# Kernel optimization log

Measured on AMD Instinct MI355X. Metric: run time of the kernel, lower is better.

The kernel has to match this reference:

```python
import jax, jax.numpy as jnp
import numpy as np

EPS = 1e-5

def setup_inputs() -> dict:
    key = jax.random.key(0)
    k1, k2 = jax.random.split(key)
    N, D = 8192, 256
    q_features = jax.random.normal(k1, (N, D), dtype=jnp.float32)
    g_features = jax.random.normal(k2, (N, D), dtype=jnp.float32)
    return {"q_features": q_features, "g_features": g_features}

def reference(q_features, g_features):
    # logits[i, j] = q_i . g_j ; original computes row i as g_features @ q_i
    logits = jnp.einsum('id,jd->ij', q_features, g_features)  # [N, N]
    # exp(l_ii)/sum_j exp(l_ij) == softmax row diagonal (stable form, same math)
    probs_diag = jnp.diagonal(jax.nn.softmax(logits, axis=-1))  # [N]
    loss = jnp.mean(-jnp.log(probs_diag + EPS))
    return loss
```

## Files before the change

### kernel.cpp

```cpp
#include <hip/hip_runtime.h>
#include <stdint.h>


#define LOG2E 1.44269504f
#define KOFF  92.3324826f

typedef __attribute__((ext_vector_type(4))) float f32x4;
typedef __attribute__((ext_vector_type(4))) int   i32x4;
typedef __attribute__((ext_vector_type(8))) int   i32x8;

typedef __attribute__((address_space(1))) const uint32_t gu32;
typedef __attribute__((address_space(3))) uint32_t lu32;

static __device__ __forceinline__ i32x8 cat8(i32x4 lo, i32x4 hi) {
    i32x8 r;
    r[0] = lo[0]; r[1] = lo[1]; r[2] = lo[2]; r[3] = lo[3];
    r[4] = hi[0]; r[5] = hi[1]; r[6] = hi[2]; r[7] = hi[3];
    return r;
}

__global__ __launch_bounds__(256) void k_cvt(const float* __restrict__ q,
                                             const float* __restrict__ g,
                                             char* __restrict__ qb,
                                             char* __restrict__ gb) {
    int o = blockIdx.x * 256 + threadIdx.x;
    const float* src = q;
    char* dst = qb;
    float sc = LOG2E;
    if (o >= 262144) { o -= 262144; src = g; dst = gb; sc = 1.0f; }
    int row = o >> 5, slot = o & 31;
    const float4* sp = (const float4*)(src + row * 256 + slot * 8);
    float4 a = sp[0], b = sp[1];
    uint32_t w0 = __builtin_amdgcn_cvt_pk_fp8_f32(a.x * sc, a.y * sc, 0, false);
    w0 = __builtin_amdgcn_cvt_pk_fp8_f32(a.z * sc, a.w * sc, w0, true);
    uint32_t w1 = __builtin_amdgcn_cvt_pk_fp8_f32(b.x * sc, b.y * sc, 0, false);
    w1 = __builtin_amdgcn_cvt_pk_fp8_f32(b.z * sc, b.w * sc, w1, true);
    int p = row >> 6, cf = (row >> 4) & 3, l15 = row & 15;
    int kb = slot >> 4;
    int gi = slot & 15;
    int quad = gi >> 2;
    int j = gi & 3;
    uint2 wv; wv.x = w0; wv.y = w1;
    *(uint2*)(dst + (size_t)p * 16384 + ((kb * 4 + cf) << 11)
              + ((j >> 1) << 10) + (quad * 16 + l15) * 16 + (j & 1) * 8) = wv;
}

__global__ __launch_bounds__(512, 2) void k_main(const char* __restrict__ qb,
                                                 const char* __restrict__ gb,
                                                 float* __restrict__ zpart,
                                                 float* __restrict__ diag) {
    __shared__ char lds[16384];
    const int tid  = threadIdx.x;
    const int wave = tid >> 6;
    const int lane = tid & 63;
    const int l15  = lane & 15;
    const int quad = lane >> 4;
    const int h2   = wave & 1;
    const int t    = blockIdx.x >> 5;
    const int cs   = blockIdx.x & 31;
    const int rowbase = t * 256 + wave * 32;

    i32x8 afrag[2][2];
    {
        const char* qp = qb + (size_t)(t * 4 + (wave >> 1)) * 16384 + lane * 16;
#pragma unroll
        for (int rg = 0; rg < 2; ++rg)
#pragma unroll
            for (int kb = 0; kb < 2; ++kb) {
                const char* tp = qp + ((kb * 4 + h2 * 2 + rg) << 11);
                afrag[rg][kb] = cat8(*(const i32x4*)tp, *(const i32x4*)(tp + 1024));
            }
    }

    float zacc[2][4];
#pragma unroll
    for (int rg = 0; rg < 2; ++rg)
#pragma unroll
        for (int r = 0; r < 4; ++r) zacc[rg][r] = 0.f;

    const bool bd = (t == cs);

    for (int jt = 0; jt < 4; ++jt) {
        const char* gp = gb + (size_t)(cs * 4 + jt) * 16384;
#pragma unroll
        for (int i = 0; i < 2; ++i) {
            int c = wave * 2 + i;
            __builtin_amdgcn_global_load_lds(
                (gu32*)(gp + (c << 10) + (lane << 4)),
                (lu32*)(lds + (c << 10)), 16, 0, 0);
        }
        __syncthreads();

        const bool dg = bd && (jt == (wave >> 1));
#pragma unroll
        for (int cf = 0; cf < 4; ++cf) {
            f32x4 acc[2];
#pragma unroll
            for (int rg = 0; rg < 2; ++rg)
                acc[rg] = (f32x4){-KOFF, -KOFF, -KOFF, -KOFF};
#pragma unroll
            for (int kb = 0; kb < 2; ++kb) {
                const char* bp = lds + ((kb * 4 + cf) << 11) + lane * 16;
                i32x8 b = cat8(*(const i32x4*)bp, *(const i32x4*)(bp + 1024));
#pragma unroll
                for (int rg = 0; rg < 2; ++rg)
                    acc[rg] = __builtin_amdgcn_mfma_scale_f32_16x16x128_f8f6f4(
                        afrag[rg][kb], b, acc[rg],
                        0, 0,
                        0, 0x7f7f7f7f,
                        0, 0x7f7f7f7f);
            }
#pragma unroll
            for (int rg = 0; rg < 2; ++rg)
#pragma unroll
                for (int r = 0; r < 4; ++r)
                    zacc[rg][r] += __builtin_amdgcn_exp2f(acc[rg][r]);
            if (dg) {
                int rgd = cf - h2 * 2;
                if (rgd >= 0 && rgd < 2) {
#pragma unroll
                    for (int r = 0; r < 4; ++r)
                        if (quad * 4 + r == l15)
                            diag[rowbase + rgd * 16 + l15] = acc[rgd][r];
                }
            }
        }
        __syncthreads();
    }

#pragma unroll
    for (int d = 1; d < 16; d <<= 1)
#pragma unroll
        for (int rg = 0; rg < 2; ++rg)
#pragma unroll
            for (int r = 0; r < 4; ++r)
                zacc[rg][r] += __shfl_xor(zacc[rg][r], d, 64);

    if (l15 == 0) {
#pragma unroll
        for (int rg = 0; rg < 2; ++rg)
#pragma unroll
            for (int r = 0; r < 4; ++r)
                zpart[(rowbase + rg * 16 + quad * 4 + r) * 32 + cs] = zacc[rg][r];
    }
}

__global__ __launch_bounds__(256) void k_fin1(const float* __restrict__ zpart,
                                              const float* __restrict__ diag,
                                              float* __restrict__ partial) {
    __shared__ float red[4];
    int r = blockIdx.x * 256 + threadIdx.x;
    const float4* z = (const float4*)(zpart + r * 32);
    float Z = 0.f;
#pragma unroll
    for (int i = 0; i < 8; ++i) {
        float4 a = z[i];
        Z += (a.x + a.y) + (a.z + a.w);
    }
    float p = __builtin_amdgcn_exp2f(diag[r]) / Z;
    float v = -logf(p + 1e-5f);
#pragma unroll
    for (int dd = 1; dd < 64; dd <<= 1) v += __shfl_xor(v, dd, 64);
    if ((threadIdx.x & 63) == 0) red[threadIdx.x >> 6] = v;
    __syncthreads();
    if (threadIdx.x == 0)
        partial[blockIdx.x] = (red[0] + red[1]) + (red[2] + red[3]);
}

__global__ void k_fin2(const float* __restrict__ partial, float* __restrict__ out) {
    float v = (threadIdx.x < 32) ? partial[threadIdx.x] : 0.f;
#pragma unroll
    for (int d = 1; d < 32; d <<= 1) v += __shfl_xor(v, d, 64);
    if (threadIdx.x == 0) out[0] = v * (1.f / 8192.f);
}

extern "C" void kernel_launch(void* const* d_in, const int* in_sizes, int n_in,
                              void* d_out, int out_size, void* d_ws, size_t ws_size,
                              hipStream_t stream) {
    const float* q = (const float*)d_in[0];
    const float* g = (const float*)d_in[1];
    char* ws = (char*)d_ws;
    char*  qb     = ws;
    char*  gb     = ws + (2u << 20);
    float* diag   = (float*)(ws + (4u << 20));
    float* zpart  = (float*)(ws + (4u << 20) + (32u << 10));
    float* partial= (float*)(ws + (4u << 20) + (1056u << 10));
    k_cvt <<<2048, 256, 0, stream>>>(q, g, qb, gb);
    k_main<<<1024, 512, 0, stream>>>(qb, gb, zpart, diag);
    k_fin1<<<32,   256, 0, stream>>>(zpart, diag, partial);
    k_fin2<<<1,     64, 0, stream>>>(partial, (float*)d_out);
    (void)in_sizes; (void)n_in; (void)out_size; (void)ws_size;
}
```

Measured before the change: 96.17 us.

## Double-buffer LDS tiles in main kernel and merge final reduction kernels

Doubles the shared-memory buffer in the main GEMM+exp kernel so the next g tile's global-to-LDS load is issued before computing on the current tile, overlapping load latency with MFMA work and dropping one barrier per iteration. The two tail reduction kernels are merged into one using an atomic counter, reset in the conversion kernel, so the last block performs the final sum. This removes one kernel launch. LDS use per block doubles to 32KB, which may affect occupancy at two blocks per CU.

```diff
diff --git a/kernel.cpp b/kernel.cpp
--- a/kernel.cpp
+++ b/kernel.cpp
@@ -22,7 +22,9 @@
 __global__ __launch_bounds__(256) void k_cvt(const float* __restrict__ q,
                                              const float* __restrict__ g,
                                              char* __restrict__ qb,
-                                             char* __restrict__ gb) {
+                                             char* __restrict__ gb,
+                                             unsigned* __restrict__ counter) {
+    if (blockIdx.x == 0 && threadIdx.x == 0) *counter = 0u;
     int o = blockIdx.x * 256 + threadIdx.x;
     const float* src = q;
     char* dst = qb;
@@ -49,7 +51,7 @@
                                                  const char* __restrict__ gb,
                                                  float* __restrict__ zpart,
                                                  float* __restrict__ diag) {
-    __shared__ char lds[16384];
+    __shared__ char lds[2][16384];
     const int tid  = threadIdx.x;
     const int wave = tid >> 6;
     const int lane = tid & 63;
@@ -80,18 +82,28 @@
 
     const bool bd = (t == cs);
 
+    const char* gbase = gb + (size_t)(cs * 4) * 16384;
+#define STAGE(JT, BUF)                                                        \
+    {                                                                         \
+        const char* gp = gbase + (size_t)(JT) * 16384;                        \
+        _Pragma("unroll")                                                     \
+        for (int i = 0; i < 2; ++i) {                                         \
+            int c = wave * 2 + i;                                             \
+            __builtin_amdgcn_global_load_lds(                                 \
+                (gu32*)(gp + (c << 10) + (lane << 4)),                        \
+                (lu32*)(&lds[BUF][0] + (c << 10)), 16, 0, 0);                 \
+        }                                                                     \
+    }
+
+    STAGE(0, 0);
+    __syncthreads();
+    int cur = 0;
+
     for (int jt = 0; jt < 4; ++jt) {
-        const char* gp = gb + (size_t)(cs * 4 + jt) * 16384;
-#pragma unroll
-        for (int i = 0; i < 2; ++i) {
-            int c = wave * 2 + i;
-            __builtin_amdgcn_global_load_lds(
-                (gu32*)(gp + (c << 10) + (lane << 4)),
-                (lu32*)(lds + (c << 10)), 16, 0, 0);
-        }
-        __syncthreads();
+        if (jt < 3) STAGE(jt + 1, cur ^ 1);
 
         const bool dg = bd && (jt == (wave >> 1));
+        const char* lbase = &lds[cur][0];
 #pragma unroll
         for (int cf = 0; cf < 4; ++cf) {
             f32x4 acc[2];
@@ -100,7 +112,7 @@
                 acc[rg] = (f32x4){-KOFF, -KOFF, -KOFF, -KOFF};
 #pragma unroll
             for (int kb = 0; kb < 2; ++kb) {
-                const char* bp = lds + ((kb * 4 + cf) << 11) + lane * 16;
+                const char* bp = lbase + ((kb * 4 + cf) << 11) + lane * 16;
                 i32x8 b = cat8(*(const i32x4*)bp, *(const i32x4*)(bp + 1024));
 #pragma unroll
                 for (int rg = 0; rg < 2; ++rg)
@@ -125,8 +137,12 @@
                 }
             }
         }
-        __syncthreads();
-    }
+        if (jt < 3) {
+            __syncthreads();
+            cur ^= 1;
+        }
+    }
+#undef STAGE
 
 #pragma unroll
     for (int d = 1; d < 16; d <<= 1)
@@ -145,10 +161,13 @@
     }
 }
 
-__global__ __launch_bounds__(256) void k_fin1(const float* __restrict__ zpart,
-                                              const float* __restrict__ diag,
-                                              float* __restrict__ partial) {
+__global__ __launch_bounds__(256) void k_fin(const float* __restrict__ zpart,
+                                             const float* __restrict__ diag,
+                                             float* __restrict__ partial,
+                                             unsigned* __restrict__ counter,
+                                             float* __restrict__ out) {
     __shared__ float red[4];
+    __shared__ int lastflag;
     int r = blockIdx.x * 256 + threadIdx.x;
     const float4* z = (const float4*)(zpart + r * 32);
     float Z = 0.f;
@@ -163,15 +182,26 @@
     for (int dd = 1; dd < 64; dd <<= 1) v += __shfl_xor(v, dd, 64);
     if ((threadIdx.x & 63) == 0) red[threadIdx.x >> 6] = v;
     __syncthreads();
-    if (threadIdx.x == 0)
-        partial[blockIdx.x] = (red[0] + red[1]) + (red[2] + red[3]);
-}
-
-__global__ void k_fin2(const float* __restrict__ partial, float* __restrict__ out) {
-    float v = (threadIdx.x < 32) ? partial[threadIdx.x] : 0.f;
-#pragma unroll
-    for (int d = 1; d < 32; d <<= 1) v += __shfl_xor(v, d, 64);
-    if (threadIdx.x == 0) out[0] = v * (1.f / 8192.f);
+    if (threadIdx.x == 0) {
+        float bsum = (red[0] + red[1]) + (red[2] + red[3]);
+        __hip_atomic_store(&partial[blockIdx.x], bsum,
+                           __ATOMIC_RELAXED, __HIP_MEMORY_SCOPE_AGENT);
+        __threadfence();
+        lastflag = (atomicAdd(counter, 1u) == 31u);
+    }
+    __syncthreads();
+    if (lastflag) {
+        __threadfence();
+        float v2 = 0.f;
+        if (threadIdx.x < 32)
+            v2 = __hip_atomic_load(&partial[threadIdx.x],
+                                   __ATOMIC_RELAXED, __HIP_MEMORY_SCOPE_AGENT);
+        if (threadIdx.x < 64) {
+#pragma unroll
+            for (int d = 1; d < 32; d <<= 1) v2 += __shfl_xor(v2, d, 64);
+            if (threadIdx.x == 0) out[0] = v2 * (1.f / 8192.f);
+        }
+    }
 }
 
 extern "C" void kernel_launch(void* const* d_in, const int* in_sizes, int n_in,
@@ -185,9 +215,9 @@
     float* diag   = (float*)(ws + (4u << 20));
     float* zpart  = (float*)(ws + (4u << 20) + (32u << 10));
     float* partial= (float*)(ws + (4u << 20) + (1056u << 10));
-    k_cvt <<<2048, 256, 0, stream>>>(q, g, qb, gb);
+    unsigned* ctr = (unsigned*)(ws + (4u << 20) + (1056u << 10) + 128);
+    k_cvt <<<2048, 256, 0, stream>>>(q, g, qb, gb, ctr);
     k_main<<<1024, 512, 0, stream>>>(qb, gb, zpart, diag);
-    k_fin1<<<32,   256, 0, stream>>>(zpart, diag, partial);
-    k_fin2<<<1,     64, 0, stream>>>(partial, (float*)d_out);
+    k_fin <<<32,   256, 0, stream>>>(zpart, diag, partial, ctr, (float*)d_out);
     (void)in_sizes; (void)n_in; (void)out_size; (void)ws_size;
 }
```

Result: faster. 93.58 us (-2.7%).
